# Kernel optimization log

Measured on AMD Instinct MI355X. Metric: run time of the kernel, lower is better.

The kernel has to match this reference:

```python
import jax, jax.numpy as jnp
import numpy as np

D_MODEL = 1024
N_HEADS = 32
HEAD_DIM = D_MODEL // N_HEADS
EPS = 1e-5


def setup_inputs() -> dict:
    key = jax.random.key(0)
    ks = jax.random.split(key, 6)
    B, S = 2, 2048
    scale = 1.0 / np.sqrt(D_MODEL)
    return {
        "x": jax.random.normal(ks[0], (B, S, D_MODEL), dtype=jnp.float32),
        "Wqkv_w": jax.random.normal(ks[1], (3 * D_MODEL, D_MODEL), dtype=jnp.float32) * scale,
        "Wqkv_b": jax.random.normal(ks[2], (3 * D_MODEL,), dtype=jnp.float32) * 0.01,
        "gn_w": jnp.ones((D_MODEL,), dtype=jnp.float32),
        "gn_b": jnp.zeros((D_MODEL,), dtype=jnp.float32),
        "out_w": jax.random.normal(ks[3], (D_MODEL, D_MODEL), dtype=jnp.float32) * scale,
        "out_b": jax.random.normal(ks[4], (D_MODEL,), dtype=jnp.float32) * 0.01,
    }


def reference(x, Wqkv_w, Wqkv_b, gn_w, gn_b, out_w, out_b):
    B, S, Dm = x.shape
    H, Dh = N_HEADS, HEAD_DIM
    # QKV projection
    qkv = x @ Wqkv_w.T + Wqkv_b                      # [B,S,3*Dm]
    qkv = qkv.reshape(B, S, 3, H, Dh)
    q, k, v = qkv[:, :, 0], qkv[:, :, 1], qkv[:, :, 2]  # each [B,S,H,Dh]
    # Linear (softmax-free) attention; dropout p=0 -> identity
    a = jnp.einsum('bthd,bshd->bhts', q, k)          # [B,H,S,S]
    ctx = jnp.einsum('bhts,bshd->bthd', a, v)        # [B,S,H,Dh]
    # GroupNorm(num_groups=H, num_channels=Dm) on transposed (B, Dm, S):
    # normalizes jointly over (Dh channels, S positions) per (batch, group)
    g = ctx.transpose(0, 2, 3, 1)                    # [B,H,Dh,S]
    mean = g.mean(axis=(2, 3), keepdims=True)
    var = ((g - mean) ** 2).mean(axis=(2, 3), keepdims=True)
    gh = (g - mean) * jax.lax.rsqrt(var + EPS)
    gh = gh * gn_w.reshape(H, Dh, 1) + gn_b.reshape(H, Dh, 1)
    ctx = gh.transpose(0, 3, 1, 2).reshape(B, S, Dm)  # back to [B,S,Dm]
    return ctx @ out_w.T + out_b
```

## Files before the change

### kernel.cpp

```cpp
#include <hip/hip_runtime.h>
#include <hip/hip_bf16.h>
#include <stdint.h>

typedef unsigned short ushort_t;
typedef __attribute__((ext_vector_type(4))) float f32x4;
typedef __attribute__((ext_vector_type(8))) short short8;

#define SS 2048
#define ROWS 4096
#define EPS 1e-5f

__device__ __forceinline__ unsigned short f2bf(float f) {
  unsigned int u = __float_as_uint(f);
  u += 0x7FFF + ((u >> 16) & 1);
  return (unsigned short)(u >> 16);
}
__device__ __forceinline__ float bf2f(short s) {
  return __uint_as_float(((unsigned int)(unsigned short)s) << 16);
}

#define GLDS16(g, l)                                                        \
  __builtin_amdgcn_global_load_lds((__attribute__((address_space(1))) void*)(g), \
                                   (__attribute__((address_space(3))) void*)(l), 16, 0, 0)

__global__ __launch_bounds__(256) void f2b3_kernel(const float* __restrict__ a,
                                                   ushort_t* __restrict__ oa, int n4a,
                                                   const float* __restrict__ b,
                                                   ushort_t* __restrict__ ob, int n4b,
                                                   const float* __restrict__ c,
                                                   ushort_t* __restrict__ oc, int n4c) {
  const int stride = gridDim.x * blockDim.x;
  const int total = n4a + n4b + n4c;
  for (int i = blockIdx.x * blockDim.x + threadIdx.x; i < total; i += stride) {
    const float* src; ushort_t* dst; int idx;
    if (i < n4a)            { src = a; dst = oa; idx = i; }
    else if (i < n4a + n4b) { src = b; dst = ob; idx = i - n4a; }
    else                    { src = c; dst = oc; idx = i - n4a - n4b; }
    const float4 v = reinterpret_cast<const float4*>(src)[idx];
    ushort4 o;
    o.x = f2bf(v.x); o.y = f2bf(v.y); o.z = f2bf(v.z); o.w = f2bf(v.w);
    reinterpret_cast<ushort4*>(dst)[idx] = o;
  }
}

#define MF(d, va, vb) d = __builtin_amdgcn_mfma_f32_16x16x32_bf16(va, vb, d, 0, 0, 0)
#define LD8(p) (*reinterpret_cast<const short8*>(p))

__global__ __launch_bounds__(512, 2) void gemm1_pipe(const ushort_t* __restrict__ A,
                                                     const ushort_t* __restrict__ B,
                                                     const float* __restrict__ bias,
                                                     ushort_t* __restrict__ C) {
  __shared__ __align__(16) ushort_t lds[4 * 14336];
  const int tid = threadIdx.x;
  const int wid = tid >> 6, lane = tid & 63;
  const int bm = blockIdx.x * 256, bn = blockIdx.y * 192;
  const int wm = wid >> 2, wn = wid & 3;

  const int srow = lane >> 2;
  const int scol = ((lane & 3) ^ ((lane >> 3) & 3)) * 8;
  const int widb = (wid < 6) ? wid : 0;
  const ushort_t* gA0 = A + (size_t)(bm + wid * 16 + srow) * 1024 + scol;
  const ushort_t* gA1 = A + (size_t)(bm + (8 + wid) * 16 + srow) * 1024 + scol;
  const ushort_t* gB0 = B + (size_t)(bn + widb * 16 + srow) * 1024 + scol;
  const ushort_t* gB1 = B + (size_t)(bn + (6 + widb) * 16 + srow) * 1024 + scol;

  const int lf = lane & 15, kf = lane >> 4;
  const int flip = ((lane >> 1) & 3) << 4;
  const int aBase = (((wm * 128 + lf) * 64 + kf * 16) ^ flip) >> 1;
  const int bBase = ((((wn * 48 + lf) * 64 + kf * 16) ^ flip) >> 1) + 8192;

  f32x4 acc[8][3] = {};

#define STAGE_A(t)                                                           \
  { ushort_t* d = lds + (((t) & 3) * 14336);                                 \
    GLDS16(gA0 + (t) * 32, d + wid * 512);                                   \
    GLDS16(gA1 + (t) * 32, d + (8 + wid) * 512); }
#define STAGE_B(t)                                                           \
  if (wid < 6) { ushort_t* d = lds + (((t) & 3) * 14336) + 8192;             \
    GLDS16(gB0 + (t) * 32, d + wid * 512);                                   \
    GLDS16(gB1 + (t) * 32, d + (6 + wid) * 512); }

  STAGE_A(0) STAGE_B(0)
  STAGE_A(1) STAGE_B(1)
  STAGE_A(2) STAGE_B(2)
  if (wid < 6) { asm volatile("s_waitcnt vmcnt(8)" ::: "memory"); }
  else         { asm volatile("s_waitcnt vmcnt(4)" ::: "memory"); }
  __builtin_amdgcn_s_barrier();
  __builtin_amdgcn_sched_barrier(0);

#define K_TILE(t, DO_STAGE, VM6, VM2)                                        \
  { const ushort_t* Lb = lds + (((t) & 3) * 14336);                          \
    short8 bv0 = LD8(Lb + bBase);                                            \
    short8 bv1 = LD8(Lb + bBase + 512);                                      \
    short8 bv2 = LD8(Lb + bBase + 1024);                                     \
    short8 a0 = LD8(Lb + aBase);                                             \
    short8 a1 = LD8(Lb + aBase + 512);                                       \
    short8 a2 = LD8(Lb + aBase + 1024);                                      \
    short8 a3 = LD8(Lb + aBase + 1536);                                      \
    if (DO_STAGE) STAGE_A((t) + 3)                                           \
    __builtin_amdgcn_s_setprio(1);                                           \
    MF(acc[0][0], a0, bv0); MF(acc[1][0], a1, bv0);                          \
    MF(acc[0][1], a0, bv1); MF(acc[1][1], a1, bv1);                          \
    MF(acc[0][2], a0, bv2); MF(acc[1][2], a1, bv2);                          \
    MF(acc[2][0], a2, bv0); MF(acc[3][0], a3, bv0);                          \
    MF(acc[2][1], a2, bv1); MF(acc[3][1], a3, bv1);                          \
    MF(acc[2][2], a2, bv2); MF(acc[3][2], a3, bv2);                          \
    __builtin_amdgcn_s_setprio(0);                                           \
    a0 = LD8(Lb + aBase + 2048);                                             \
    a1 = LD8(Lb + aBase + 2560);                                             \
    a2 = LD8(Lb + aBase + 3072);                                             \
    a3 = LD8(Lb + aBase + 3584);                                             \
    if (DO_STAGE) STAGE_B((t) + 3)                                           \
    __builtin_amdgcn_s_setprio(1);                                           \
    MF(acc[4][0], a0, bv0); MF(acc[5][0], a1, bv0);                          \
    MF(acc[4][1], a0, bv1); MF(acc[5][1], a1, bv1);                          \
    MF(acc[4][2], a0, bv2); MF(acc[5][2], a1, bv2);                          \
    MF(acc[6][0], a2, bv0); MF(acc[7][0], a3, bv0);                          \
    MF(acc[6][1], a2, bv1); MF(acc[7][1], a3, bv1);                          \
    MF(acc[6][2], a2, bv2); MF(acc[7][2], a3, bv2);                          \
    __builtin_amdgcn_s_setprio(0);                                           \
    __builtin_amdgcn_sched_barrier(0);                                       \
    if (wid < 6) { asm volatile("s_waitcnt vmcnt(" #VM6 ")" ::: "memory"); } \
    else         { asm volatile("s_waitcnt vmcnt(" #VM2 ")" ::: "memory"); } \
    __builtin_amdgcn_s_barrier();                                            \
    __builtin_amdgcn_sched_barrier(0); }

#pragma unroll 1
  for (int t = 0; t < 29; ++t) K_TILE(t, 1, 8, 4)
  K_TILE(29, 0, 4, 2)
  K_TILE(30, 0, 0, 0)
  K_TILE(31, 0, 0, 0)

  const int crow = bm + wm * 128 + (lane >> 4) * 4;
  const int ccol = bn + wn * 48 + (lane & 15);
#pragma unroll
  for (int m = 0; m < 8; ++m)
#pragma unroll
    for (int n = 0; n < 3; ++n) {
      const int col = ccol + n * 16;
      const float bb = bias[col];
#pragma unroll
      for (int j = 0; j < 4; ++j)
        C[(size_t)(crow + m * 16 + j) * 3072 + col] = f2bf(acc[m][n][j] + bb);
    }
#undef K_TILE
#undef STAGE_A
#undef STAGE_B
}

__global__ __launch_bounds__(256, 2) void gemm2_pipe(const ushort_t* __restrict__ A,
                                                     const ushort_t* __restrict__ B,
                                                     const float* __restrict__ bias,
                                                     float* __restrict__ C) {
  __shared__ __align__(16) ushort_t lds[4 * 6144];
  const int tid = threadIdx.x;
  const int wid = tid >> 6, lane = tid & 63;
  const int bm = blockIdx.x * 64, bn = blockIdx.y * 128;
  const int wm = wid >> 1, wn = wid & 1;

  const int srow = lane >> 2;
  const int scol = ((lane & 3) ^ ((lane >> 3) & 3)) * 8;
  const ushort_t* gA  = A + (size_t)(bm + wid * 16 + srow) * 1024 + scol;
  const ushort_t* gB0 = B + (size_t)(bn + wid * 16 + srow) * 1024 + scol;
  const ushort_t* gB1 = B + (size_t)(bn + (4 + wid) * 16 + srow) * 1024 + scol;

  const int lf = lane & 15, kf = lane >> 4;
  const int flip = ((lane >> 1) & 3) << 4;
  const int aBase = (((wm * 32 + lf) * 64 + kf * 16) ^ flip) >> 1;
  const int bBase = ((((wn * 64 + lf) * 64 + kf * 16) ^ flip) >> 1) + 2048;

  f32x4 acc[2][4] = {};

#define STAGE2(t)                                                            \
  { ushort_t* d = lds + (((t) & 3) * 6144);                                  \
    GLDS16(gA + (t) * 32, d + wid * 512);                                    \
    GLDS16(gB0 + (t) * 32, d + 2048 + wid * 512);                            \
    GLDS16(gB1 + (t) * 32, d + 2048 + (4 + wid) * 512); }

  STAGE2(0) STAGE2(1) STAGE2(2)
  asm volatile("s_waitcnt vmcnt(6)" ::: "memory");
  __builtin_amdgcn_s_barrier();
  __builtin_amdgcn_sched_barrier(0);

#define K_TILE2(t, DO_STAGE, VM)                                             \
  { const ushort_t* Lb = lds + (((t) & 3) * 6144);                           \
    short8 bv0 = LD8(Lb + bBase);                                            \
    short8 bv1 = LD8(Lb + bBase + 512);                                      \
    short8 bv2 = LD8(Lb + bBase + 1024);                                     \
    short8 bv3 = LD8(Lb + bBase + 1536);                                     \
    short8 a0 = LD8(Lb + aBase);                                             \
    short8 a1 = LD8(Lb + aBase + 512);                                       \
    if (DO_STAGE) STAGE2((t) + 3)                                            \
    __builtin_amdgcn_s_setprio(1);                                           \
    MF(acc[0][0], a0, bv0); MF(acc[1][0], a1, bv0);                          \
    MF(acc[0][1], a0, bv1); MF(acc[1][1], a1, bv1);                          \
    MF(acc[0][2], a0, bv2); MF(acc[1][2], a1, bv2);                          \
    MF(acc[0][3], a0, bv3); MF(acc[1][3], a1, bv3);                          \
    __builtin_amdgcn_s_setprio(0);                                           \
    __builtin_amdgcn_sched_barrier(0);                                       \
    asm volatile("s_waitcnt vmcnt(" #VM ")" ::: "memory");                   \
    __builtin_amdgcn_s_barrier();                                            \
    __builtin_amdgcn_sched_barrier(0); }

#pragma unroll 1
  for (int t = 0; t < 29; ++t) K_TILE2(t, 1, 6)
  K_TILE2(29, 0, 3)
  K_TILE2(30, 0, 0)
  K_TILE2(31, 0, 0)

  const int crow = bm + wm * 32 + (lane >> 4) * 4;
  const int ccol = bn + wn * 64 + lf;
#pragma unroll
  for (int m = 0; m < 2; ++m)
#pragma unroll
    for (int n = 0; n < 4; ++n) {
      const int col = ccol + n * 16;
      const float bb = bias[col];
#pragma unroll
      for (int j = 0; j < 4; ++j)
        C[(size_t)(crow + m * 16 + j) * 1024 + col] = acc[m][n][j] + bb;
    }
#undef K_TILE2
#undef STAGE2
}

__global__ __launch_bounds__(256) void kvq_partial(const ushort_t* __restrict__ qkvb,
                                                   float* __restrict__ KVp,
                                                   float* __restrict__ Qcovp,
                                                   float* __restrict__ qsump) {
  __shared__ float qt[64 * 32];
  __shared__ float kt[64 * 32];
  __shared__ float vt[64 * 32];
  const int blk = blockIdx.x;
  const int bh = blk >> 5;
  const int ch = blk & 31;
  const int b = bh >> 5, h = bh & 31;
  const int tid = threadIdx.x;
  const int r = tid >> 2, cg = (tid & 3) * 8;
  const ushort_t* base = qkvb + (size_t)(b * SS + ch * 64 + r) * 3072 + h * 32 + cg;
  const short8 q8 = LD8(base);
  const short8 k8 = LD8(base + 1024);
  const short8 v8 = LD8(base + 2048);
#pragma unroll
  for (int i = 0; i < 8; ++i) {
    qt[r * 32 + cg + i] = bf2f(q8[i]);
    kt[r * 32 + cg + i] = bf2f(k8[i]);
    vt[r * 32 + cg + i] = bf2f(v8[i]);
  }
  __syncthreads();
  const int d = tid & 31, eg = tid >> 5;
  float kv[4] = {0.f, 0.f, 0.f, 0.f};
  float qc[4] = {0.f, 0.f, 0.f, 0.f};
#pragma unroll 4
  for (int ss = 0; ss < 64; ++ss) {
    const float vv = vt[ss * 32 + d];
    const float qd = qt[ss * 32 + d];
#pragma unroll
    for (int i = 0; i < 4; ++i) {
      kv[i] += kt[ss * 32 + eg * 4 + i] * vv;
      qc[i] += qt[ss * 32 + eg * 4 + i] * qd;
    }
  }
  float* okv = KVp + ((size_t)bh * 32 + ch) * 1024 + (eg * 4) * 32 + d;
  float* oqc = Qcovp + ((size_t)bh * 32 + ch) * 1024 + (eg * 4) * 32 + d;
#pragma unroll
  for (int i = 0; i < 4; ++i) { okv[i * 32] = kv[i]; oqc[i * 32] = qc[i]; }
  if (tid < 32) {
    float s = 0.f;
    for (int ss = 0; ss < 64; ++ss) s += qt[ss * 32 + tid];
    qsump[((size_t)bh * 32 + ch) * 32 + tid] = s;
  }
}

__global__ __launch_bounds__(256) void ctx_norm_kernel(const ushort_t* __restrict__ qkvb,
                                                       const float* __restrict__ KVp,
                                                       const float* __restrict__ Qcovp,
                                                       const float* __restrict__ qsump,
                                                       const float* __restrict__ gw,
                                                       const float* __restrict__ gb,
                                                       ushort_t* __restrict__ ghb) {
  __shared__ float kvs[1024], qcov[1024];
  __shared__ float qsums[32], gws[32], gbs[32];
  __shared__ float red[16];
  __shared__ float sstats[2];
  const int blk = blockIdx.x;
  const int bh = blk >> 3, tt = blk & 7;
  const int b = bh >> 5, h = bh & 31;
  const int tid = threadIdx.x;
  {
    const float* kbase = KVp + (size_t)bh * 32768 + tid * 4;
    const float* qbase = Qcovp + (size_t)bh * 32768 + tid * 4;
    float4 sk = make_float4(0.f, 0.f, 0.f, 0.f);
    float4 sq = make_float4(0.f, 0.f, 0.f, 0.f);
    for (int c = 0; c < 32; ++c) {
      const float4 k4 = *(const float4*)(kbase + c * 1024);
      const float4 q4 = *(const float4*)(qbase + c * 1024);
      sk.x += k4.x; sk.y += k4.y; sk.z += k4.z; sk.w += k4.w;
      sq.x += q4.x; sq.y += q4.y; sq.z += q4.z; sq.w += q4.w;
    }
    *(float4*)&kvs[tid * 4] = sk;
    *(float4*)&qcov[tid * 4] = sq;
  }
  if (tid < 32) {
    float s = 0.f;
    for (int c = 0; c < 32; ++c) s += qsump[((size_t)bh * 32 + c) * 32 + tid];
    qsums[tid] = s;
    gws[tid] = gw[h * 32 + tid];
    gbs[tid] = gb[h * 32 + tid];
  }
  __syncthreads();
  {
    const int d = tid & 31, ig = tid >> 5;
    float e2p = 0.f;
#pragma unroll
    for (int ii = 0; ii < 4; ++ii) {
      const int i = ig * 4 + ii;
      float t = 0.f;
#pragma unroll
      for (int j = 0; j < 32; ++j) t += qcov[i * 32 + j] * kvs[j * 32 + d];
      e2p += kvs[i * 32 + d] * t;
    }
#pragma unroll
    for (int off = 32; off > 0; off >>= 1) e2p += __shfl_down(e2p, off);
    float mp = 0.f;
    if (tid < 32) {
      float rs = 0.f;
      for (int dd = 0; dd < 32; ++dd) rs += kvs[tid * 32 + ((dd + tid) & 31)];
      mp = rs * qsums[tid];
    }
#pragma unroll
    for (int off = 32; off > 0; off >>= 1) mp += __shfl_down(mp, off);
    const int wave = tid >> 6, lane = tid & 63;
    if (lane == 0) { red[wave] = e2p; red[8 + wave] = mp; }
    __syncthreads();
    if (tid == 0) {
      const float E2 = red[0] + red[1] + red[2] + red[3];
      const float MS = red[8] + red[9] + red[10] + red[11];
      const float mean = MS * (1.f / 65536.f);
      const float var = E2 * (1.f / 65536.f) - mean * mean;
      sstats[0] = mean;
      sstats[1] = rsqrtf(var + EPS);
    }
    __syncthreads();
  }
  const float mean = sstats[0], rstd = sstats[1];
  const int t = tt * 256 + tid;
  const ushort_t* qrow = qkvb + ((size_t)(b * SS + t)) * 3072 + h * 32;
  float q[32];
#pragma unroll
  for (int g = 0; g < 4; ++g) {
    const short8 qv = LD8(qrow + g * 8);
#pragma unroll
    for (int i = 0; i < 8; ++i) q[g * 8 + i] = bf2f(qv[i]);
  }
  float o[32];
#pragma unroll
  for (int d = 0; d < 32; ++d) o[d] = 0.f;
#pragma unroll
  for (int e = 0; e < 32; ++e) {
    const float qe = q[e];
    const float* kr = &kvs[e * 32];
#pragma unroll
    for (int d = 0; d < 32; ++d) o[d] += qe * kr[d];
  }
  ushort_t* crow = ghb + ((size_t)(b * SS + t)) * 1024 + h * 32;
#pragma unroll
  for (int g = 0; g < 4; ++g) {
    short8 ov;
#pragma unroll
    for (int i = 0; i < 8; ++i) {
      const int d = g * 8 + i;
      ov[i] = (short)f2bf((o[d] - mean) * rstd * gws[d] + gbs[d]);
    }
    *(short8*)(crow + g * 8) = ov;
  }
}

extern "C" void kernel_launch(void* const* d_in, const int* in_sizes, int n_in,
                              void* d_out, int out_size, void* d_ws, size_t ws_size,
                              hipStream_t stream) {
  const float* x  = (const float*)d_in[0];
  const float* w1 = (const float*)d_in[1];
  const float* b1 = (const float*)d_in[2];
  const float* gw = (const float*)d_in[3];
  const float* gb = (const float*)d_in[4];
  const float* w2 = (const float*)d_in[5];
  const float* b2 = (const float*)d_in[6];
  float* out = (float*)d_out;

  char* ws = (char*)d_ws;
  ushort_t* Xb    = (ushort_t*)(ws);
  float*    KVp   = (float*)(ws);
  ushort_t* W1b   = (ushort_t*)(ws + 8388608);
  float*    Qcovp = (float*)(ws + 8388608);
  ushort_t* qkvb  = (ushort_t*)(ws + 16777216);
  ushort_t* ghb   = (ushort_t*)(ws + 41943040);
  ushort_t* W2b   = (ushort_t*)(ws + 50331648);
  float*    qsump = (float*)(ws + 52428800);

  f2b3_kernel<<<2048, 256, 0, stream>>>(x, Xb, ROWS * 1024 / 4,
                                        w1, W1b, 3072 * 1024 / 4,
                                        w2, W2b, 1024 * 1024 / 4);
  gemm1_pipe<<<dim3(16, 16), 512, 0, stream>>>(Xb, W1b, b1, qkvb);
  kvq_partial<<<2048, 256, 0, stream>>>(qkvb, KVp, Qcovp, qsump);
  ctx_norm_kernel<<<512, 256, 0, stream>>>(qkvb, KVp, Qcovp, qsump, gw, gb, ghb);
  gemm2_pipe<<<dim3(64, 8), 256, 0, stream>>>(ghb, W2b, b2, out);
}
```

Before: 103.5 us.

## Split KV reduction and stats into own kernel; remap GEMM1 blocks per XCD

Before this change, each of the 8 ctx_norm blocks per (batch, head) redundantly reduced 32 KV/Qcov partials and recomputed the GroupNorm statistics. That work now runs once per (batch, head) in a new 64-block kernel, and ctx_norm only loads the reduced KV and a mean/rstd pair. GEMM1 block indices are also remapped so blocks sharing A/B tiles land on the same XCD for better L2 reuse. The cost is an extra launch and a small low-occupancy kernel on the critical path.

New measurement: 93.45 us. 1.11x faster.

```diff
diff --git a/kernel.cpp b/kernel.cpp
--- a/kernel.cpp
+++ b/kernel.cpp
@@ -53,7 +53,10 @@
   __shared__ __align__(16) ushort_t lds[4 * 14336];
   const int tid = threadIdx.x;
   const int wid = tid >> 6, lane = tid & 63;
-  const int bm = blockIdx.x * 256, bn = blockIdx.y * 192;
+  const int lin = blockIdx.x + (blockIdx.y << 4);
+  const int xcd = lin & 7, idx = lin >> 3;
+  const int bm = (((xcd & 3) << 2) + (idx & 3)) * 256;
+  const int bn = (((xcd >> 2) << 3) + (idx >> 2)) * 192;
   const int wm = wid >> 2, wn = wid & 3;
 
   const int srow = lane >> 2;
@@ -272,20 +275,13 @@
   }
 }
 
-__global__ __launch_bounds__(256) void ctx_norm_kernel(const ushort_t* __restrict__ qkvb,
-                                                       const float* __restrict__ KVp,
-                                                       const float* __restrict__ Qcovp,
-                                                       const float* __restrict__ qsump,
-                                                       const float* __restrict__ gw,
-                                                       const float* __restrict__ gb,
-                                                       ushort_t* __restrict__ ghb) {
-  __shared__ float kvs[1024], qcov[1024];
-  __shared__ float qsums[32], gws[32], gbs[32];
-  __shared__ float red[16];
-  __shared__ float sstats[2];
-  const int blk = blockIdx.x;
-  const int bh = blk >> 3, tt = blk & 7;
-  const int b = bh >> 5, h = bh & 31;
+__global__ __launch_bounds__(256) void kvq_reduce_stats(const float* __restrict__ KVp,
+                                                        const float* __restrict__ Qcovp,
+                                                        const float* __restrict__ qsump,
+                                                        float* __restrict__ KV,
+                                                        float2* __restrict__ stats) {
+  __shared__ float kvs[1024], qcov[1024], qsums[32], red[16];
+  const int bh = blockIdx.x;
   const int tid = threadIdx.x;
   {
     const float* kbase = KVp + (size_t)bh * 32768 + tid * 4;
@@ -300,50 +296,63 @@
     }
     *(float4*)&kvs[tid * 4] = sk;
     *(float4*)&qcov[tid * 4] = sq;
+    *(float4*)&KV[(size_t)bh * 1024 + tid * 4] = sk;
   }
   if (tid < 32) {
     float s = 0.f;
     for (int c = 0; c < 32; ++c) s += qsump[((size_t)bh * 32 + c) * 32 + tid];
     qsums[tid] = s;
-    gws[tid] = gw[h * 32 + tid];
-    gbs[tid] = gb[h * 32 + tid];
   }
   __syncthreads();
-  {
-    const int d = tid & 31, ig = tid >> 5;
-    float e2p = 0.f;
-#pragma unroll
-    for (int ii = 0; ii < 4; ++ii) {
-      const int i = ig * 4 + ii;
-      float t = 0.f;
-#pragma unroll
-      for (int j = 0; j < 32; ++j) t += qcov[i * 32 + j] * kvs[j * 32 + d];
-      e2p += kvs[i * 32 + d] * t;
-    }
-#pragma unroll
-    for (int off = 32; off > 0; off >>= 1) e2p += __shfl_down(e2p, off);
-    float mp = 0.f;
-    if (tid < 32) {
-      float rs = 0.f;
-      for (int dd = 0; dd < 32; ++dd) rs += kvs[tid * 32 + ((dd + tid) & 31)];
-      mp = rs * qsums[tid];
-    }
-#pragma unroll
-    for (int off = 32; off > 0; off >>= 1) mp += __shfl_down(mp, off);
-    const int wave = tid >> 6, lane = tid & 63;
-    if (lane == 0) { red[wave] = e2p; red[8 + wave] = mp; }
-    __syncthreads();
-    if (tid == 0) {
-      const float E2 = red[0] + red[1] + red[2] + red[3];
-      const float MS = red[8] + red[9] + red[10] + red[11];
-      const float mean = MS * (1.f / 65536.f);
-      const float var = E2 * (1.f / 65536.f) - mean * mean;
-      sstats[0] = mean;
-      sstats[1] = rsqrtf(var + EPS);
-    }
-    __syncthreads();
-  }
-  const float mean = sstats[0], rstd = sstats[1];
+  const int d = tid & 31, ig = tid >> 5;
+  float e2p = 0.f;
+#pragma unroll
+  for (int ii = 0; ii < 4; ++ii) {
+    const int i = ig * 4 + ii;
+    float t = 0.f;
+#pragma unroll
+    for (int j = 0; j < 32; ++j) t += qcov[i * 32 + j] * kvs[j * 32 + d];
+    e2p += kvs[i * 32 + d] * t;
+  }
+#pragma unroll
+  for (int off = 32; off > 0; off >>= 1) e2p += __shfl_down(e2p, off);
+  float mp = 0.f;
+  if (tid < 32) {
+    float rs = 0.f;
+    for (int dd = 0; dd < 32; ++dd) rs += kvs[tid * 32 + ((dd + tid) & 31)];
+    mp = rs * qsums[tid];
+  }
+#pragma unroll
+  for (int off = 32; off > 0; off >>= 1) mp += __shfl_down(mp, off);
+  const int wave = tid >> 6, lane = tid & 63;
+  if (lane == 0) { red[wave] = e2p; red[8 + wave] = mp; }
+  __syncthreads();
+  if (tid == 0) {
+    const float E2 = red[0] + red[1] + red[2] + red[3];
+    const float MS = red[8] + red[9] + red[10] + red[11];
+    const float mean = MS * (1.f / 65536.f);
+    const float var = E2 * (1.f / 65536.f) - mean * mean;
+    stats[bh] = make_float2(mean, rsqrtf(var + EPS));
+  }
+}
+
+__global__ __launch_bounds__(256) void ctx_norm_kernel(const ushort_t* __restrict__ qkvb,
+                                                       const float* __restrict__ KV,
+                                                       const float2* __restrict__ stats,
+                                                       const float* __restrict__ gw,
+                                                       const float* __restrict__ gb,
+                                                       ushort_t* __restrict__ ghb) {
+  __shared__ float kvs[1024];
+  __shared__ float gws[32], gbs[32];
+  const int blk = blockIdx.x;
+  const int bh = blk >> 3, tt = blk & 7;
+  const int b = bh >> 5, h = bh & 31;
+  const int tid = threadIdx.x;
+  for (int i = tid; i < 1024; i += 256) kvs[i] = KV[(size_t)bh * 1024 + i];
+  if (tid < 32) { gws[tid] = gw[h * 32 + tid]; gbs[tid] = gb[h * 32 + tid]; }
+  const float2 st = stats[bh];
+  __syncthreads();
+  const float mean = st.x, rstd = st.y;
   const int t = tt * 256 + tid;
   const ushort_t* qrow = qkvb + ((size_t)(b * SS + t)) * 3072 + h * 32;
   float q[32];
@@ -397,12 +406,15 @@
   ushort_t* ghb   = (ushort_t*)(ws + 41943040);
   ushort_t* W2b   = (ushort_t*)(ws + 50331648);
   float*    qsump = (float*)(ws + 52428800);
+  float*    KV    = (float*)(ws + 52690944);
+  float2*   stats = (float2*)(ws + 52953088);
 
   f2b3_kernel<<<2048, 256, 0, stream>>>(x, Xb, ROWS * 1024 / 4,
                                         w1, W1b, 3072 * 1024 / 4,
                                         w2, W2b, 1024 * 1024 / 4);
   gemm1_pipe<<<dim3(16, 16), 512, 0, stream>>>(Xb, W1b, b1, qkvb);
   kvq_partial<<<2048, 256, 0, stream>>>(qkvb, KVp, Qcovp, qsump);
-  ctx_norm_kernel<<<512, 256, 0, stream>>>(qkvb, KVp, Qcovp, qsump, gw, gb, ghb);
+  kvq_reduce_stats<<<64, 256, 0, stream>>>(KVp, Qcovp, qsump, KV, stats);
+  ctx_norm_kernel<<<512, 256, 0, stream>>>(qkvb, KV, stats, gw, gb, ghb);
   gemm2_pipe<<<dim3(64, 8), 256, 0, stream>>>(ghb, W2b, b2, out);
 }
```
